# Optimization experiments

Measured on AMD Instinct MI355X. Metric: run time of the kernel, lower is better.

The kernel has to match this reference:

```python
import jax, jax.numpy as jnp
import numpy as np
import math

N_EMBED = 1024
N_HEAD = 16
BLOCK_SIZE = 2048

def setup_inputs() -> dict:
    key = jax.random.key(0)
    k1, k2, k3, k4, k5 = jax.random.split(key, 5)
    s = 0.02
    x = jax.random.normal(k1, (2, 2048, N_EMBED), dtype=jnp.float32)
    W_qkv = jax.random.normal(k2, (N_EMBED, 3 * N_EMBED), dtype=jnp.float32) * s
    b_qkv = jax.random.normal(k3, (3 * N_EMBED,), dtype=jnp.float32) * s
    W_out = jax.random.normal(k4, (N_EMBED, N_EMBED), dtype=jnp.float32) * s
    b_out = jax.random.normal(k5, (N_EMBED,), dtype=jnp.float32) * s
    return {"x": x, "W_qkv": W_qkv, "b_qkv": b_qkv, "W_out": W_out, "b_out": b_out}

def reference(x, W_qkv, b_qkv, W_out, b_out):
    b, s, d = x.shape
    hd = d // N_HEAD  # head dim
    qkv = x @ W_qkv + b_qkv                       # [b, s, 3d]
    q, k, v = jnp.split(qkv, 3, axis=-1)
    # [b, h, s, hd]
    q = q.reshape(b, s, N_HEAD, hd).transpose(0, 2, 1, 3)
    k = k.reshape(b, s, N_HEAD, hd).transpose(0, 2, 1, 3)
    v = v.reshape(b, s, N_HEAD, hd).transpose(0, 2, 1, 3)
    scale = 1.0 / math.sqrt(hd)
    sims = jnp.einsum('bhqd,bhkd->bhqk', q, k) * scale  # [b, h, s, s]
    causal = jnp.tril(jnp.ones((s, s), dtype=bool))
    sims = jnp.where(causal[None, None], sims, -jnp.inf)
    probs = jax.nn.softmax(sims, axis=-1)
    attn = jnp.einsum('bhqk,bhkd->bhqd', probs, v)       # [b, h, s, hd]
    attn = attn.transpose(0, 2, 1, 3).reshape(b, s, d)
    return attn @ W_out + b_out
```

## Files before the change

kernel.cpp:

```cpp
#include <hip/hip_runtime.h>
#include <hip/hip_bf16.h>

typedef __attribute__((ext_vector_type(8))) short short8;
typedef __attribute__((ext_vector_type(4))) short short4v;
typedef __attribute__((ext_vector_type(4))) float f32x4;
typedef __attribute__((ext_vector_type(16))) float f32x16;
typedef __attribute__((ext_vector_type(4))) unsigned int u32x4;
typedef unsigned short u16;

__device__ __forceinline__ u16 f2bf(float f) {
  __hip_bfloat16 h = __float2bfloat16(f);
  return __builtin_bit_cast(unsigned short, h);
}

__device__ __forceinline__ unsigned pack2(float lo, float hi) {
  return (unsigned)f2bf(lo) | ((unsigned)f2bf(hi) << 16);
}

__device__ __forceinline__ void gload16(const u16* g, u16* l) {
  __builtin_amdgcn_global_load_lds(
      (const __attribute__((address_space(1))) unsigned int*)g,
      (__attribute__((address_space(3))) unsigned int*)l, 16, 0, 0);
}

__global__ void prep_kernel(const float* __restrict__ x,
                            const float* __restrict__ Wqkv,
                            const float* __restrict__ Wout,
                            u16* __restrict__ Xb,
                            u16* __restrict__ WqkvT,
                            u16* __restrict__ WoutT) {
  __shared__ float tile[32][33];
  const int b = blockIdx.x, tid = threadIdx.x;
  if (b < 4096) {
    const int i = (b * 256 + tid) * 4;
    float4 f = *(const float4*)(x + i);
    uint2 pk;
    pk.x = pack2(f.x, f.y);
    pk.y = pack2(f.z, f.w);
    *(uint2*)(Xb + i) = pk;
    return;
  }
  const float* in;
  u16* out;
  int N, bx, by;
  if (b < 7168) {
    in = Wqkv; out = WqkvT; N = 3072;
    const int bb = b - 4096;
    bx = bb % 96; by = bb / 96;
  } else {
    in = Wout; out = WoutT; N = 1024;
    const int bb = b - 7168;
    bx = bb % 32; by = bb / 32;
  }
  const int n0 = bx * 32, k0 = by * 32;
  const int tx = tid & 31, ty = tid >> 5;
#pragma unroll
  for (int r = 0; r < 4; ++r) {
    const int k = ty + r * 8;
    tile[k][tx] = in[(size_t)(k0 + k) * N + n0 + tx];
  }
  __syncthreads();
#pragma unroll
  for (int r = 0; r < 4; ++r) {
    const int n = ty + r * 8;
    out[(size_t)(n0 + n) * 1024 + k0 + tx] = f2bf(tile[tx][n]);
  }
}

template <int EPI, int BN>
__global__ __launch_bounds__(256, 2) void gemm_kernel(const u16* __restrict__ A,
                                                      const u16* __restrict__ Bt,
                                                      const float* __restrict__ bias,
                                                      void* __restrict__ outp) {
  __shared__ u16 Al[128 * 64];
  __shared__ u16 Bl[BN * 64];
  constexpr int NF = BN / 32;
  const int tid = threadIdx.x;
  const int lane = tid & 63, wid = tid >> 6;
  const int l15 = lane & 15, lg = lane >> 4;
  const int wm = wid >> 1, wn = wid & 1;
  const int m0 = blockIdx.y * 128, n0 = blockIdx.x * BN;

  f32x4 acc[4][NF] = {};

  for (int k0 = 0; k0 < 1024; k0 += 64) {
    __syncthreads();
#pragma unroll
    for (int i = 0; i < 4; ++i) {
      const int p = i * 4096 + tid * 16;
      const int row = p >> 7;
      const int lslot = ((p >> 4) & 7) ^ (row & 7);
      gload16(A + (size_t)(m0 + row) * 1024 + k0 + lslot * 8, Al + i * 2048 + wid * 512);
    }
#pragma unroll
    for (int i = 0; i < NF; ++i) {
      const int p = i * 4096 + tid * 16;
      const int row = p >> 7;
      const int lslot = ((p >> 4) & 7) ^ (row & 7);
      gload16(Bt + (size_t)(n0 + row) * 1024 + k0 + lslot * 8, Bl + i * 2048 + wid * 512);
    }
    __syncthreads();
#pragma unroll
    for (int ks = 0; ks < 2; ++ks) {
      short8 af[4], bfr[NF];
#pragma unroll
      for (int m = 0; m < 4; ++m) {
        const int row = wm * 64 + m * 16 + l15;
        af[m] = *(const short8*)((const char*)Al + row * 128 + (((ks * 4 + lg) ^ (row & 7)) << 4));
      }
#pragma unroll
      for (int n = 0; n < NF; ++n) {
        const int row = wn * (BN / 2) + n * 16 + l15;
        bfr[n] = *(const short8*)((const char*)Bl + row * 128 + (((ks * 4 + lg) ^ (row & 7)) << 4));
      }
#pragma unroll
      for (int m = 0; m < 4; ++m)
#pragma unroll
        for (int n = 0; n < NF; ++n)
          acc[m][n] = __builtin_amdgcn_mfma_f32_16x16x32_bf16(af[m], bfr[n], acc[m][n], 0, 0, 0);
    }
  }

  if (EPI == 0) {
    u16* qkv = (u16*)outp;
#pragma unroll
    for (int m = 0; m < 4; ++m)
#pragma unroll
      for (int n = 0; n < NF; ++n) {
        const int gcol = n0 + wn * (BN / 2) + n * 16 + l15;
        const int which = gcol >> 10, dd = gcol & 1023;
        const int h = dd >> 6, hd = dd & 63;
        const float bb = bias[gcol];
        const int grow0 = m0 + wm * 64 + m * 16 + lg * 4;
        const int b = grow0 >> 11, s0 = grow0 & 2047;
        if (which == 2) {
          const int bsub = (s0 >> 2) & 3;
          const int bper = (bsub == 1) ? 2 : (bsub == 2) ? 1 : bsub;
          const int s0p = (s0 & ~15) | (bper << 2);
          short4v pk;
#pragma unroll
          for (int j = 0; j < 4; ++j) pk[j] = (short)f2bf(acc[m][n][j] + bb);
          *(short4v*)(qkv + (size_t)2 * 4194304 + ((size_t)(b * 16 + h) * 64 + hd) * 2048 + s0p) = pk;
        } else {
          const float sc = (which == 0) ? 0.18033688011112042f : 1.0f;
#pragma unroll
          for (int j = 0; j < 4; ++j) {
            float v = (acc[m][n][j] + bb) * sc;
            qkv[(size_t)which * 4194304 + ((size_t)(b * 16 + h) * 2048 + s0 + j) * 64 + hd] = f2bf(v);
          }
        }
      }
  } else {
    float* O = (float*)outp;
#pragma unroll
    for (int m = 0; m < 4; ++m)
#pragma unroll
      for (int n = 0; n < NF; ++n) {
        const int gcol = n0 + wn * (BN / 2) + n * 16 + l15;
        const float bb = bias[gcol];
#pragma unroll
        for (int j = 0; j < 4; ++j) {
          const int grow = m0 + wm * 64 + m * 16 + lg * 4 + j;
          O[(size_t)grow * 1024 + gcol] = acc[m][n][j] + bb;
        }
      }
  }
}

__global__ __launch_bounds__(256, 2) void attn_kernel(const u16* __restrict__ Q,
                                                      const u16* __restrict__ K,
                                                      const u16* __restrict__ VT,
                                                      u16* __restrict__ Aout) {
  const int bh = blockIdx.y;
  const int p = blockIdx.x;
  const int tid = threadIdx.x, lane = tid & 63, wid = tid >> 6;
  const int l31 = lane & 31, h = lane >> 5;
  const int qs = wid & 1, kp = wid >> 1;

  __shared__ __align__(16) char smem[36864];
  u16(*Kl)[4096] = (u16(*)[4096])smem;
  u16(*Vl)[4096] = (u16(*)[4096])(smem + 16384);

  const u16* Qb = Q + (size_t)bh * 2048 * 64;
  const u16* Kb = K + (size_t)bh * 2048 * 64;
  const u16* Vb = VT + (size_t)bh * 64 * 2048;

  const int qA = p * 64 + qs * 32;
  const int qB = (31 - p) * 64 + qs * 32;
  const int R = 32 - p;

  short8 qfA[4], qfB[4];
#pragma unroll
  for (int ks = 0; ks < 4; ++ks) {
    qfA[ks] = *(const short8*)(Qb + (size_t)(qA + l31) * 64 + ks * 16 + h * 8);
    qfB[ks] = *(const short8*)(Qb + (size_t)(qB + l31) * 64 + ks * 16 + h * 8);
  }

  f32x16 accA[2] = {}, accB[2] = {};
  float mA = -1e30f, mB = -1e30f, lA = 0.f, lB = 0.f;

  auto stage = [&](int buf, size_t kb) {
#pragma unroll
    for (int i = 0; i < 2; ++i) {
      const int row = i * 32 + (tid >> 3);
      const int sc = ((tid & 7) ^ (row & 7)) * 8;
      gload16(Kb + (kb + row) * 64 + sc, &Kl[buf][i * 2048 + wid * 512]);
      gload16(Vb + (size_t)row * 2048 + kb + sc, &Vl[buf][i * 2048 + wid * 512]);
    }
  };

  stage(0, 0);
  __syncthreads();

  for (int t = 0; t < R; ++t) {
    const int cur = t & 1;
    if (t + 1 < R) stage(cur ^ 1, (size_t)(t + 1) * 64);

    const int kvbase = t * 64 + kp * 32;
    const bool actB = kvbase <= qB + 31;
    const bool actA = kvbase <= qA + 31;
    if (actB) {
      short8 kf[4], vf[2][2];
      const int krow = kp * 32 + l31;
#pragma unroll
      for (int ks = 0; ks < 4; ++ks)
        kf[ks] = *(const short8*)((const char*)&Kl[cur][0] + krow * 128 +
                                  (((ks * 2 + h) ^ (krow & 7)) << 4));
#pragma unroll
      for (int n = 0; n < 2; ++n)
#pragma unroll
        for (int ks = 0; ks < 2; ++ks) {
          const int row = n * 32 + l31;
          vf[n][ks] = *(const short8*)((const char*)&Vl[cur][0] + row * 128 +
                                       (((kp * 4 + ks * 2 + h) ^ (row & 7)) << 4));
        }

      f32x16 saB = {}, saA = {};
      __builtin_amdgcn_s_setprio(1);
#pragma unroll
      for (int ks = 0; ks < 4; ++ks)
        saB = __builtin_amdgcn_mfma_f32_32x32x16_bf16(kf[ks], qfB[ks], saB, 0, 0, 0);
      if (actA) {
#pragma unroll
        for (int ks = 0; ks < 4; ++ks)
          saA = __builtin_amdgcn_mfma_f32_32x32x16_bf16(kf[ks], qfA[ks], saA, 0, 0, 0);
      }
      __builtin_amdgcn_s_setprio(0);

      auto finish = [&](f32x16& sa, f32x16(&acc)[2], float& m, float& l, int q0) {
        if (kvbase == q0) {
#pragma unroll
          for (int r = 0; r < 16; ++r) {
            const int kvr = (r & 3) + 8 * (r >> 2) + 4 * h;
            if (kvr > l31) sa[r] = -1e30f;
          }
        }
        const float t0 = fmaxf(fmaxf(sa[0], sa[1]), sa[2]);
        const float t1 = fmaxf(fmaxf(sa[3], sa[4]), sa[5]);
        const float t2 = fmaxf(fmaxf(sa[6], sa[7]), sa[8]);
        const float t3 = fmaxf(fmaxf(sa[9], sa[10]), sa[11]);
        const float t4 = fmaxf(fmaxf(sa[12], sa[13]), sa[14]);
        float rm = fmaxf(fmaxf(fmaxf(t0, t1), t2), fmaxf(fmaxf(t3, t4), sa[15]));
        rm = fmaxf(rm, __shfl_xor(rm, 32));
        if (!__all(rm <= m + 5.0f)) {
          const float mn = fmaxf(m, rm);
          const float corr = exp2f(m - mn);
          m = mn;
          l *= corr;
#pragma unroll
          for (int n = 0; n < 2; ++n)
#pragma unroll
            for (int r = 0; r < 16; ++r) acc[n][r] *= corr;
        }
#pragma unroll
        for (int r = 0; r < 16; ++r) sa[r] = exp2f(sa[r] - m);
        float rs = (((sa[0] + sa[1]) + (sa[2] + sa[3])) + ((sa[4] + sa[5]) + (sa[6] + sa[7]))) +
                   (((sa[8] + sa[9]) + (sa[10] + sa[11])) + ((sa[12] + sa[13]) + (sa[14] + sa[15])));
        l += rs + __shfl_xor(rs, 32);
        unsigned c[8];
#pragma unroll
        for (int i = 0; i < 8; ++i) c[i] = pack2(sa[2 * i], sa[2 * i + 1]);
        const short8 pk0 = __builtin_bit_cast(short8, (u32x4){c[0], c[1], c[2], c[3]});
        const short8 pk1 = __builtin_bit_cast(short8, (u32x4){c[4], c[5], c[6], c[7]});
        __builtin_amdgcn_s_setprio(1);
#pragma unroll
        for (int n = 0; n < 2; ++n) {
          acc[n] = __builtin_amdgcn_mfma_f32_32x32x16_bf16(vf[n][0], pk0, acc[n], 0, 0, 0);
          acc[n] = __builtin_amdgcn_mfma_f32_32x32x16_bf16(vf[n][1], pk1, acc[n], 0, 0, 0);
        }
        __builtin_amdgcn_s_setprio(0);
      };

      finish(saB, accB, mB, lB, qB);
      if (actA) finish(saA, accA, mA, lA, qA);
    }
    __syncthreads();
  }

  float* comb = (float*)smem;
  float* pA = comb + ((qs * 2 + 0) * 64 + lane) * 36;
  float* pB = comb + ((qs * 2 + 1) * 64 + lane) * 36;
  if (kp == 1) {
    pA[0] = mA; pA[1] = lA;
    pB[0] = mB; pB[1] = lB;
#pragma unroll
    for (int n = 0; n < 2; ++n)
#pragma unroll
      for (int r = 0; r < 16; ++r) {
        pA[2 + n * 16 + r] = accA[n][r];
        pB[2 + n * 16 + r] = accB[n][r];
      }
  }
  __syncthreads();
  if (kp == 0) {
    const int b = bh >> 4, hh = bh & 15;
    auto merge_store = [&](const float* pp, const f32x16(&acc)[2], float m0, float l0, int q0) {
      const float m1 = pp[0], l1 = pp[1];
      const float mn = fmaxf(m0, m1);
      const float c0 = exp2f(m0 - mn), c1 = exp2f(m1 - mn);
      const float inv = 1.0f / (l0 * c0 + l1 * c1);
      u16* rowp = Aout + (size_t)(b * 2048 + q0 + l31) * 1024 + hh * 64;
#pragma unroll
      for (int n = 0; n < 2; ++n)
#pragma unroll
        for (int r = 0; r < 16; r += 2) {
          const int hd = n * 32 + (r & 3) + 8 * (r >> 2) + 4 * h;
          const float v0 = (acc[n][r] * c0 + pp[2 + n * 16 + r] * c1) * inv;
          const float v1 = (acc[n][r + 1] * c0 + pp[2 + n * 16 + r + 1] * c1) * inv;
          *(unsigned*)(rowp + hd) = pack2(v0, v1);
        }
    };
    merge_store(pA, accA, mA, lA, qA);
    merge_store(pB, accB, mB, lB, qB);
  }
}

extern "C" void kernel_launch(void* const* d_in, const int* in_sizes, int n_in,
                              void* d_out, int out_size, void* d_ws, size_t ws_size,
                              hipStream_t stream) {
  const float* x = (const float*)d_in[0];
  const float* Wqkv = (const float*)d_in[1];
  const float* bqkv = (const float*)d_in[2];
  const float* Wout = (const float*)d_in[3];
  const float* bout = (const float*)d_in[4];

  char* ws = (char*)d_ws;
  u16* Xb = (u16*)(ws + 0);
  u16* WqkvT = (u16*)(ws + 8388608);
  u16* WoutT = (u16*)(ws + 14680064);
  u16* QKV = (u16*)(ws + 16777216);
  u16* Attn = Xb;

  prep_kernel<<<8192, 256, 0, stream>>>(x, Wqkv, Wout, Xb, WqkvT, WoutT);
  gemm_kernel<0, 128><<<dim3(24, 32), 256, 0, stream>>>(Xb, WqkvT, bqkv, QKV);
  attn_kernel<<<dim3(16, 32), 256, 0, stream>>>(QKV, QKV + 4194304, QKV + 8388608, Attn);
  gemm_kernel<1, 64><<<dim3(16, 32), 256, 0, stream>>>(Attn, WoutT, bout, d_out);
}
```

Before: 102.0 us.

## Split attention KV range across four wave pairs with 512-thread blocks

The attention block grows from 256 to 512 threads, so four KV splits (kp 0..3) process two 64-row KV tiles per round instead of two splits over one tile. The loop count per block roughly halves and more waves are available to hide latency. In exchange, shared memory doubles to 64 KB for the double-buffered K/V, and the final softmax merge becomes a three-step serialized reduction with extra barriers. Occupancy may drop because of the larger LDS footprint and register pressure.

New measurement: 272.3 us. +166.9%, slower.

```diff
diff --git a/kernel.cpp b/kernel.cpp
--- a/kernel.cpp
+++ b/kernel.cpp
@@ -167,7 +167,7 @@
   }
 }
 
-__global__ __launch_bounds__(256, 2) void attn_kernel(const u16* __restrict__ Q,
+__global__ __launch_bounds__(512, 4) void attn_kernel(const u16* __restrict__ Q,
                                                       const u16* __restrict__ K,
                                                       const u16* __restrict__ VT,
                                                       u16* __restrict__ Aout) {
@@ -176,10 +176,11 @@
   const int tid = threadIdx.x, lane = tid & 63, wid = tid >> 6;
   const int l31 = lane & 31, h = lane >> 5;
   const int qs = wid & 1, kp = wid >> 1;
-
-  __shared__ __align__(16) char smem[36864];
-  u16(*Kl)[4096] = (u16(*)[4096])smem;
-  u16(*Vl)[4096] = (u16(*)[4096])(smem + 16384);
+  const int jt = kp >> 1, sub = kp & 1;
+
+  __shared__ __align__(16) char smem[65536];
+  u16(*Kl)[8192] = (u16(*)[8192])smem;
+  u16(*Vl)[8192] = (u16(*)[8192])(smem + 32768);
 
   const u16* Qb = Q + (size_t)bh * 2048 * 64;
   const u16* Kb = K + (size_t)bh * 2048 * 64;
@@ -188,6 +189,7 @@
   const int qA = p * 64 + qs * 32;
   const int qB = (31 - p) * 64 + qs * 32;
   const int R = 32 - p;
+  const int ROUNDS = (R + 1) >> 1;
 
   short8 qfA[4], qfB[4];
 #pragma unroll
@@ -199,40 +201,43 @@
   f32x16 accA[2] = {}, accB[2] = {};
   float mA = -1e30f, mB = -1e30f, lA = 0.f, lB = 0.f;
 
-  auto stage = [&](int buf, size_t kb) {
-#pragma unroll
-    for (int i = 0; i < 2; ++i) {
-      const int row = i * 32 + (tid >> 3);
-      const int sc = ((tid & 7) ^ (row & 7)) * 8;
-      gload16(Kb + (kb + row) * 64 + sc, &Kl[buf][i * 2048 + wid * 512]);
-      gload16(Vb + (size_t)row * 2048 + kb + sc, &Vl[buf][i * 2048 + wid * 512]);
+  const int srow = tid >> 3;
+  const int ssc = ((tid & 7) ^ (srow & 7)) * 8;
+  auto stage = [&](int buf, size_t kb, int nt) {
+    for (int i = 0; i < nt; ++i) {
+      gload16(Kb + (kb + i * 64 + srow) * 64 + ssc, &Kl[buf][i * 4096 + wid * 512]);
+      gload16(Vb + (size_t)srow * 2048 + kb + i * 64 + ssc, &Vl[buf][i * 4096 + wid * 512]);
     }
   };
 
-  stage(0, 0);
+  stage(0, 0, (R >= 2) ? 2 : 1);
   __syncthreads();
 
-  for (int t = 0; t < R; ++t) {
-    const int cur = t & 1;
-    if (t + 1 < R) stage(cur ^ 1, (size_t)(t + 1) * 64);
-
-    const int kvbase = t * 64 + kp * 32;
-    const bool actB = kvbase <= qB + 31;
-    const bool actA = kvbase <= qA + 31;
+  for (int r = 0; r < ROUNDS; ++r) {
+    const int cur = r & 1;
+    const int rem = R - 2 * (r + 1);
+    const int ntn = rem >= 2 ? 2 : (rem == 1 ? 1 : 0);
+    if (ntn > 0) stage(cur ^ 1, (size_t)(2 * (r + 1)) * 64, ntn);
+
+    const int kvbase = r * 128 + kp * 32;
+    const bool valid = (4 * r + kp) < 2 * R;
+    const bool actB = valid && kvbase <= qB + 31;
+    const bool actA = valid && kvbase <= qA + 31;
     if (actB) {
+      const char* Klt = (const char*)&Kl[cur][jt * 4096];
+      const char* Vlt = (const char*)&Vl[cur][jt * 4096];
       short8 kf[4], vf[2][2];
-      const int krow = kp * 32 + l31;
+      const int krow = sub * 32 + l31;
 #pragma unroll
       for (int ks = 0; ks < 4; ++ks)
-        kf[ks] = *(const short8*)((const char*)&Kl[cur][0] + krow * 128 +
-                                  (((ks * 2 + h) ^ (krow & 7)) << 4));
+        kf[ks] = *(const short8*)(Klt + krow * 128 + (((ks * 2 + h) ^ (krow & 7)) << 4));
 #pragma unroll
       for (int n = 0; n < 2; ++n)
 #pragma unroll
         for (int ks = 0; ks < 2; ++ks) {
           const int row = n * 32 + l31;
-          vf[n][ks] = *(const short8*)((const char*)&Vl[cur][0] + row * 128 +
-                                       (((kp * 4 + ks * 2 + h) ^ (row & 7)) << 4));
+          vf[n][ks] = *(const short8*)(Vlt + row * 128 +
+                                       (((sub * 4 + ks * 2 + h) ^ (row & 7)) << 4));
         }
 
       f32x16 saB = {}, saA = {};
@@ -250,9 +255,9 @@
       auto finish = [&](f32x16& sa, f32x16(&acc)[2], float& m, float& l, int q0) {
         if (kvbase == q0) {
 #pragma unroll
-          for (int r = 0; r < 16; ++r) {
-            const int kvr = (r & 3) + 8 * (r >> 2) + 4 * h;
-            if (kvr > l31) sa[r] = -1e30f;
+          for (int rr = 0; rr < 16; ++rr) {
+            const int kvr = (rr & 3) + 8 * (rr >> 2) + 4 * h;
+            if (kvr > l31) sa[rr] = -1e30f;
           }
         }
         const float t0 = fmaxf(fmaxf(sa[0], sa[1]), sa[2]);
@@ -270,10 +275,10 @@
 #pragma unroll
           for (int n = 0; n < 2; ++n)
 #pragma unroll
-            for (int r = 0; r < 16; ++r) acc[n][r] *= corr;
-        }
-#pragma unroll
-        for (int r = 0; r < 16; ++r) sa[r] = exp2f(sa[r] - m);
+            for (int rr = 0; rr < 16; ++rr) acc[n][rr] *= corr;
+        }
+#pragma unroll
+        for (int rr = 0; rr < 16; ++rr) sa[rr] = exp2f(sa[rr] - m);
         float rs = (((sa[0] + sa[1]) + (sa[2] + sa[3])) + ((sa[4] + sa[5]) + (sa[6] + sa[7]))) +
                    (((sa[8] + sa[9]) + (sa[10] + sa[11])) + ((sa[12] + sa[13]) + (sa[14] + sa[15])));
         l += rs + __shfl_xor(rs, 32);
@@ -297,41 +302,54 @@
     __syncthreads();
   }
 
-  float* comb = (float*)smem;
-  float* pA = comb + ((qs * 2 + 0) * 64 + lane) * 36;
-  float* pB = comb + ((qs * 2 + 1) * 64 + lane) * 36;
-  if (kp == 1) {
-    pA[0] = mA; pA[1] = lA;
-    pB[0] = mB; pB[1] = lB;
-#pragma unroll
-    for (int n = 0; n < 2; ++n)
-#pragma unroll
-      for (int r = 0; r < 16; ++r) {
-        pA[2 + n * 16 + r] = accA[n][r];
-        pB[2 + n * 16 + r] = accB[n][r];
-      }
-  }
-  __syncthreads();
+  float* pA = (float*)smem + ((qs * 2 + 0) * 64 + lane) * 36;
+  float* pB = (float*)smem + ((qs * 2 + 1) * 64 + lane) * 36;
+  for (int src = 1; src < 4; ++src) {
+    __syncthreads();
+    if (kp == src) {
+      pA[0] = mA; pA[1] = lA;
+      pB[0] = mB; pB[1] = lB;
+#pragma unroll
+      for (int n = 0; n < 2; ++n)
+#pragma unroll
+        for (int r = 0; r < 16; ++r) {
+          pA[2 + n * 16 + r] = accA[n][r];
+          pB[2 + n * 16 + r] = accB[n][r];
+        }
+    }
+    __syncthreads();
+    if (kp == 0) {
+      auto merge = [&](const float* pp, f32x16(&acc)[2], float& m, float& l) {
+        const float m1 = pp[0], l1 = pp[1];
+        const float mn = fmaxf(m, m1);
+        const float c0 = exp2f(m - mn), c1 = exp2f(m1 - mn);
+        l = l * c0 + l1 * c1;
+        m = mn;
+#pragma unroll
+        for (int n = 0; n < 2; ++n)
+#pragma unroll
+          for (int r = 0; r < 16; ++r)
+            acc[n][r] = acc[n][r] * c0 + pp[2 + n * 16 + r] * c1;
+      };
+      merge(pA, accA, mA, lA);
+      merge(pB, accB, mB, lB);
+    }
+  }
   if (kp == 0) {
     const int b = bh >> 4, hh = bh & 15;
-    auto merge_store = [&](const float* pp, const f32x16(&acc)[2], float m0, float l0, int q0) {
-      const float m1 = pp[0], l1 = pp[1];
-      const float mn = fmaxf(m0, m1);
-      const float c0 = exp2f(m0 - mn), c1 = exp2f(m1 - mn);
-      const float inv = 1.0f / (l0 * c0 + l1 * c1);
+    auto store = [&](const f32x16(&acc)[2], float l, int q0) {
+      const float inv = 1.0f / l;
       u16* rowp = Aout + (size_t)(b * 2048 + q0 + l31) * 1024 + hh * 64;
 #pragma unroll
       for (int n = 0; n < 2; ++n)
 #pragma unroll
         for (int r = 0; r < 16; r += 2) {
           const int hd = n * 32 + (r & 3) + 8 * (r >> 2) + 4 * h;
-          const float v0 = (acc[n][r] * c0 + pp[2 + n * 16 + r] * c1) * inv;
-          const float v1 = (acc[n][r + 1] * c0 + pp[2 + n * 16 + r + 1] * c1) * inv;
-          *(unsigned*)(rowp + hd) = pack2(v0, v1);
+          *(unsigned*)(rowp + hd) = pack2(acc[n][r] * inv, acc[n][r + 1] * inv);
         }
     };
-    merge_store(pA, accA, mA, lA, qA);
-    merge_store(pB, accB, mB, lB, qB);
+    store(accA, lA, qA);
+    store(accB, lB, qB);
   }
 }
 
@@ -353,6 +371,6 @@
 
   prep_kernel<<<8192, 256, 0, stream>>>(x, Wqkv, Wout, Xb, WqkvT, WoutT);
   gemm_kernel<0, 128><<<dim3(24, 32), 256, 0, stream>>>(Xb, WqkvT, bqkv, QKV);
-  attn_kernel<<<dim3(16, 32), 256, 0, stream>>>(QKV, QKV + 4194304, QKV + 8388608, Attn);
+  attn_kernel<<<dim3(16, 32), 512, 0, stream>>>(QKV, QKV + 4194304, QKV + 8388608, Attn);
   gemm_kernel<1, 64><<<dim3(16, 32), 256, 0, stream>>>(Attn, WoutT, bout, d_out);
 }
```

## Split attention workgroup into 8 waves, each handling one query tile

Applied to the files above, without the earlier changes.

The attention kernel now launches 512 threads per block instead of 256. The two paired query tiles (early and late causal tiles) are handed to separate wave groups instead of each wave processing both. K/V staging is spread over the 8 waves with one load each, and the final split-KV merge is indexed per tile. The goal is to cut per-wave serial work and register pressure so more waves hide latency. The cost is imbalance: waves on the early tile idle through most iterations while still hitting every barrier, and 8 waves share the same LDS double buffer.

New measurement: 100.2 us. About the same (-1.8%).

```diff
diff --git a/kernel.cpp b/kernel.cpp
--- a/kernel.cpp
+++ b/kernel.cpp
@@ -167,7 +167,7 @@
   }
 }
 
-__global__ __launch_bounds__(256, 2) void attn_kernel(const u16* __restrict__ Q,
+__global__ __launch_bounds__(512, 4) void attn_kernel(const u16* __restrict__ Q,
                                                       const u16* __restrict__ K,
                                                       const u16* __restrict__ VT,
                                                       u16* __restrict__ Aout) {
@@ -175,7 +175,7 @@
   const int p = blockIdx.x;
   const int tid = threadIdx.x, lane = tid & 63, wid = tid >> 6;
   const int l31 = lane & 31, h = lane >> 5;
-  const int qs = wid & 1, kp = wid >> 1;
+  const int tl = wid >> 2, qs = (wid >> 1) & 1, kp = wid & 1;
 
   __shared__ __align__(16) char smem[36864];
   u16(*Kl)[4096] = (u16(*)[4096])smem;
@@ -185,28 +185,23 @@
   const u16* Kb = K + (size_t)bh * 2048 * 64;
   const u16* Vb = VT + (size_t)bh * 64 * 2048;
 
-  const int qA = p * 64 + qs * 32;
-  const int qB = (31 - p) * 64 + qs * 32;
+  const int tile = tl ? p : (31 - p);
+  const int q0 = tile * 64 + qs * 32;
   const int R = 32 - p;
 
-  short8 qfA[4], qfB[4];
-#pragma unroll
-  for (int ks = 0; ks < 4; ++ks) {
-    qfA[ks] = *(const short8*)(Qb + (size_t)(qA + l31) * 64 + ks * 16 + h * 8);
-    qfB[ks] = *(const short8*)(Qb + (size_t)(qB + l31) * 64 + ks * 16 + h * 8);
-  }
-
-  f32x16 accA[2] = {}, accB[2] = {};
-  float mA = -1e30f, mB = -1e30f, lA = 0.f, lB = 0.f;
-
+  short8 qf[4];
+#pragma unroll
+  for (int ks = 0; ks < 4; ++ks)
+    qf[ks] = *(const short8*)(Qb + (size_t)(q0 + l31) * 64 + ks * 16 + h * 8);
+
+  f32x16 acc[2] = {};
+  float m = -1e30f, l = 0.f;
+
+  const int srow = tid >> 3;
+  const int ssc = ((tid & 7) ^ (srow & 7)) * 8;
   auto stage = [&](int buf, size_t kb) {
-#pragma unroll
-    for (int i = 0; i < 2; ++i) {
-      const int row = i * 32 + (tid >> 3);
-      const int sc = ((tid & 7) ^ (row & 7)) * 8;
-      gload16(Kb + (kb + row) * 64 + sc, &Kl[buf][i * 2048 + wid * 512]);
-      gload16(Vb + (size_t)row * 2048 + kb + sc, &Vl[buf][i * 2048 + wid * 512]);
-    }
+    gload16(Kb + (kb + srow) * 64 + ssc, &Kl[buf][wid * 512]);
+    gload16(Vb + (size_t)srow * 2048 + kb + ssc, &Vl[buf][wid * 512]);
   };
 
   stage(0, 0);
@@ -217,9 +212,7 @@
     if (t + 1 < R) stage(cur ^ 1, (size_t)(t + 1) * 64);
 
     const int kvbase = t * 64 + kp * 32;
-    const bool actB = kvbase <= qB + 31;
-    const bool actA = kvbase <= qA + 31;
-    if (actB) {
+    if (kvbase <= q0 + 31) {
       short8 kf[4], vf[2][2];
       const int krow = kp * 32 + l31;
 #pragma unroll
@@ -235,103 +228,83 @@
                                        (((kp * 4 + ks * 2 + h) ^ (row & 7)) << 4));
         }
 
-      f32x16 saB = {}, saA = {};
+      f32x16 sa = {};
       __builtin_amdgcn_s_setprio(1);
 #pragma unroll
       for (int ks = 0; ks < 4; ++ks)
-        saB = __builtin_amdgcn_mfma_f32_32x32x16_bf16(kf[ks], qfB[ks], saB, 0, 0, 0);
-      if (actA) {
-#pragma unroll
-        for (int ks = 0; ks < 4; ++ks)
-          saA = __builtin_amdgcn_mfma_f32_32x32x16_bf16(kf[ks], qfA[ks], saA, 0, 0, 0);
-      }
+        sa = __builtin_amdgcn_mfma_f32_32x32x16_bf16(kf[ks], qf[ks], sa, 0, 0, 0);
       __builtin_amdgcn_s_setprio(0);
 
-      auto finish = [&](f32x16& sa, f32x16(&acc)[2], float& m, float& l, int q0) {
-        if (kvbase == q0) {
-#pragma unroll
-          for (int r = 0; r < 16; ++r) {
-            const int kvr = (r & 3) + 8 * (r >> 2) + 4 * h;
-            if (kvr > l31) sa[r] = -1e30f;
-          }
+      if (kvbase == q0) {
+#pragma unroll
+        for (int r = 0; r < 16; ++r) {
+          const int kvr = (r & 3) + 8 * (r >> 2) + 4 * h;
+          if (kvr > l31) sa[r] = -1e30f;
         }
-        const float t0 = fmaxf(fmaxf(sa[0], sa[1]), sa[2]);
-        const float t1 = fmaxf(fmaxf(sa[3], sa[4]), sa[5]);
-        const float t2 = fmaxf(fmaxf(sa[6], sa[7]), sa[8]);
-        const float t3 = fmaxf(fmaxf(sa[9], sa[10]), sa[11]);
-        const float t4 = fmaxf(fmaxf(sa[12], sa[13]), sa[14]);
-        float rm = fmaxf(fmaxf(fmaxf(t0, t1), t2), fmaxf(fmaxf(t3, t4), sa[15]));
-        rm = fmaxf(rm, __shfl_xor(rm, 32));
-        if (!__all(rm <= m + 5.0f)) {
-          const float mn = fmaxf(m, rm);
-          const float corr = exp2f(m - mn);
-          m = mn;
-          l *= corr;
-#pragma unroll
-          for (int n = 0; n < 2; ++n)
-#pragma unroll
-            for (int r = 0; r < 16; ++r) acc[n][r] *= corr;
-        }
-#pragma unroll
-        for (int r = 0; r < 16; ++r) sa[r] = exp2f(sa[r] - m);
-        float rs = (((sa[0] + sa[1]) + (sa[2] + sa[3])) + ((sa[4] + sa[5]) + (sa[6] + sa[7]))) +
-                   (((sa[8] + sa[9]) + (sa[10] + sa[11])) + ((sa[12] + sa[13]) + (sa[14] + sa[15])));
-        l += rs + __shfl_xor(rs, 32);
-        unsigned c[8];
-#pragma unroll
-        for (int i = 0; i < 8; ++i) c[i] = pack2(sa[2 * i], sa[2 * i + 1]);
-        const short8 pk0 = __builtin_bit_cast(short8, (u32x4){c[0], c[1], c[2], c[3]});
-        const short8 pk1 = __builtin_bit_cast(short8, (u32x4){c[4], c[5], c[6], c[7]});
-        __builtin_amdgcn_s_setprio(1);
-#pragma unroll
-        for (int n = 0; n < 2; ++n) {
-          acc[n] = __builtin_amdgcn_mfma_f32_32x32x16_bf16(vf[n][0], pk0, acc[n], 0, 0, 0);
-          acc[n] = __builtin_amdgcn_mfma_f32_32x32x16_bf16(vf[n][1], pk1, acc[n], 0, 0, 0);
-        }
-        __builtin_amdgcn_s_setprio(0);
-      };
-
-      finish(saB, accB, mB, lB, qB);
-      if (actA) finish(saA, accA, mA, lA, qA);
+      }
+      const float t0 = fmaxf(fmaxf(sa[0], sa[1]), sa[2]);
+      const float t1 = fmaxf(fmaxf(sa[3], sa[4]), sa[5]);
+      const float t2 = fmaxf(fmaxf(sa[6], sa[7]), sa[8]);
+      const float t3 = fmaxf(fmaxf(sa[9], sa[10]), sa[11]);
+      const float t4 = fmaxf(fmaxf(sa[12], sa[13]), sa[14]);
+      float rm = fmaxf(fmaxf(fmaxf(t0, t1), t2), fmaxf(fmaxf(t3, t4), sa[15]));
+      rm = fmaxf(rm, __shfl_xor(rm, 32));
+      if (!__all(rm <= m + 5.0f)) {
+        const float mn = fmaxf(m, rm);
+        const float corr = exp2f(m - mn);
+        m = mn;
+        l *= corr;
+#pragma unroll
+        for (int n = 0; n < 2; ++n)
+#pragma unroll
+          for (int r = 0; r < 16; ++r) acc[n][r] *= corr;
+      }
+#pragma unroll
+      for (int r = 0; r < 16; ++r) sa[r] = exp2f(sa[r] - m);
+      float rs = (((sa[0] + sa[1]) + (sa[2] + sa[3])) + ((sa[4] + sa[5]) + (sa[6] + sa[7]))) +
+                 (((sa[8] + sa[9]) + (sa[10] + sa[11])) + ((sa[12] + sa[13]) + (sa[14] + sa[15])));
+      l += rs + __shfl_xor(rs, 32);
+      unsigned c[8];
+#pragma unroll
+      for (int i = 0; i < 8; ++i) c[i] = pack2(sa[2 * i], sa[2 * i + 1]);
+      const short8 pk0 = __builtin_bit_cast(short8, (u32x4){c[0], c[1], c[2], c[3]});
+      const short8 pk1 = __builtin_bit_cast(short8, (u32x4){c[4], c[5], c[6], c[7]});
+      __builtin_amdgcn_s_setprio(1);
+#pragma unroll
+      for (int n = 0; n < 2; ++n) {
+        acc[n] = __builtin_amdgcn_mfma_f32_32x32x16_bf16(vf[n][0], pk0, acc[n], 0, 0, 0);
+        acc[n] = __builtin_amdgcn_mfma_f32_32x32x16_bf16(vf[n][1], pk1, acc[n], 0, 0, 0);
+      }
+      __builtin_amdgcn_s_setprio(0);
     }
     __syncthreads();
   }
 
-  float* comb = (float*)smem;
-  float* pA = comb + ((qs * 2 + 0) * 64 + lane) * 36;
-  float* pB = comb + ((qs * 2 + 1) * 64 + lane) * 36;
+  float* pp = (float*)smem + (((tl << 1) | qs) * 64 + lane) * 36;
   if (kp == 1) {
-    pA[0] = mA; pA[1] = lA;
-    pB[0] = mB; pB[1] = lB;
+    pp[0] = m; pp[1] = l;
 #pragma unroll
     for (int n = 0; n < 2; ++n)
 #pragma unroll
-      for (int r = 0; r < 16; ++r) {
-        pA[2 + n * 16 + r] = accA[n][r];
-        pB[2 + n * 16 + r] = accB[n][r];
-      }
+      for (int r = 0; r < 16; ++r) pp[2 + n * 16 + r] = acc[n][r];
   }
   __syncthreads();
   if (kp == 0) {
     const int b = bh >> 4, hh = bh & 15;
-    auto merge_store = [&](const float* pp, const f32x16(&acc)[2], float m0, float l0, int q0) {
-      const float m1 = pp[0], l1 = pp[1];
-      const float mn = fmaxf(m0, m1);
-      const float c0 = exp2f(m0 - mn), c1 = exp2f(m1 - mn);
-      const float inv = 1.0f / (l0 * c0 + l1 * c1);
-      u16* rowp = Aout + (size_t)(b * 2048 + q0 + l31) * 1024 + hh * 64;
-#pragma unroll
-      for (int n = 0; n < 2; ++n)
-#pragma unroll
-        for (int r = 0; r < 16; r += 2) {
-          const int hd = n * 32 + (r & 3) + 8 * (r >> 2) + 4 * h;
-          const float v0 = (acc[n][r] * c0 + pp[2 + n * 16 + r] * c1) * inv;
-          const float v1 = (acc[n][r + 1] * c0 + pp[2 + n * 16 + r + 1] * c1) * inv;
-          *(unsigned*)(rowp + hd) = pack2(v0, v1);
-        }
-    };
-    merge_store(pA, accA, mA, lA, qA);
-    merge_store(pB, accB, mB, lB, qB);
+    const float m1 = pp[0], l1 = pp[1];
+    const float mn = fmaxf(m, m1);
+    const float c0 = exp2f(m - mn), c1 = exp2f(m1 - mn);
+    const float inv = 1.0f / (l * c0 + l1 * c1);
+    u16* rowp = Aout + (size_t)(b * 2048 + q0 + l31) * 1024 + hh * 64;
+#pragma unroll
+    for (int n = 0; n < 2; ++n)
+#pragma unroll
+      for (int r = 0; r < 16; r += 2) {
+        const int hd = n * 32 + (r & 3) + 8 * (r >> 2) + 4 * h;
+        const float v0 = (acc[n][r] * c0 + pp[2 + n * 16 + r] * c1) * inv;
+        const float v1 = (acc[n][r + 1] * c0 + pp[2 + n * 16 + r + 1] * c1) * inv;
+        *(unsigned*)(rowp + hd) = pack2(v0, v1);
+      }
   }
 }
 
@@ -353,6 +326,6 @@
 
   prep_kernel<<<8192, 256, 0, stream>>>(x, Wqkv, Wout, Xb, WqkvT, WoutT);
   gemm_kernel<0, 128><<<dim3(24, 32), 256, 0, stream>>>(Xb, WqkvT, bqkv, QKV);
-  attn_kernel<<<dim3(16, 32), 256, 0, stream>>>(QKV, QKV + 4194304, QKV + 8388608, Attn);
+  attn_kernel<<<dim3(16, 32), 512, 0, stream>>>(QKV, QKV + 4194304, QKV + 8388608, Attn);
   gemm_kernel<1, 64><<<dim3(16, 32), 256, 0, stream>>>(Attn, WoutT, bout, d_out);
 }
```

## Give each wave private K/V LDS buffers and drop per-iteration block barriers

Applied to the files above, without the earlier changes.

Each of the four waves now stages only the 32-row K/V slice it consumes into its own double-buffered LDS region. It then waits on its own loads with an explicit vmcnt instead of a workgroup __syncthreads every iteration. This removes the block-wide barrier from the attention inner loop and lets waves progress independently. The cost is LDS growing from 36 KB to 64 KB per block, which may limit the two-blocks-per-CU occupancy target, plus duplicated K loads across the qs waves.

Measured after the change: 108.2 us. +6.0%, slower.

```diff
diff --git a/kernel.cpp b/kernel.cpp
--- a/kernel.cpp
+++ b/kernel.cpp
@@ -177,9 +177,8 @@
   const int l31 = lane & 31, h = lane >> 5;
   const int qs = wid & 1, kp = wid >> 1;
 
-  __shared__ __align__(16) char smem[36864];
-  u16(*Kl)[4096] = (u16(*)[4096])smem;
-  u16(*Vl)[4096] = (u16(*)[4096])(smem + 16384);
+  __shared__ __align__(16) char smem[65536];
+  u16* wbase = (u16*)smem + wid * 8192;
 
   const u16* Qb = Q + (size_t)bh * 2048 * 64;
   const u16* Kb = K + (size_t)bh * 2048 * 64;
@@ -199,41 +198,46 @@
   f32x16 accA[2] = {}, accB[2] = {};
   float mA = -1e30f, mB = -1e30f, lA = 0.f, lB = 0.f;
 
-  auto stage = [&](int buf, size_t kb) {
-#pragma unroll
-    for (int i = 0; i < 2; ++i) {
-      const int row = i * 32 + (tid >> 3);
-      const int sc = ((tid & 7) ^ (row & 7)) * 8;
-      gload16(Kb + (kb + row) * 64 + sc, &Kl[buf][i * 2048 + wid * 512]);
-      gload16(Vb + (size_t)row * 2048 + kb + sc, &Vl[buf][i * 2048 + wid * 512]);
-    }
+  auto stage = [&](int buf, int t) {
+    const size_t kb = (size_t)t * 64 + kp * 32;
+    u16* dst = wbase + buf * 4096;
+#pragma unroll
+    for (int i = 0; i < 4; ++i) {
+      const int row = i * 8 + (lane >> 3);
+      const int g = (lane & 7) ^ (row & 7);
+      gload16(Kb + (kb + row) * 64 + g * 8, dst + i * 512);
+    }
+#pragma unroll
+    for (int i = 0; i < 4; ++i)
+      gload16(Vb + (size_t)lane * 2048 + kb + i * 8, dst + 2048 + i * 512);
   };
 
   stage(0, 0);
-  __syncthreads();
 
   for (int t = 0; t < R; ++t) {
     const int cur = t & 1;
-    if (t + 1 < R) stage(cur ^ 1, (size_t)(t + 1) * 64);
+    if (t + 1 < R) {
+      stage(cur ^ 1, t + 1);
+      asm volatile("s_waitcnt vmcnt(8)" ::: "memory");
+    } else {
+      asm volatile("s_waitcnt vmcnt(0)" ::: "memory");
+    }
+    __builtin_amdgcn_sched_barrier(0);
 
     const int kvbase = t * 64 + kp * 32;
     const bool actB = kvbase <= qB + 31;
     const bool actA = kvbase <= qA + 31;
     if (actB) {
+      const u16* cb = wbase + cur * 4096;
       short8 kf[4], vf[2][2];
-      const int krow = kp * 32 + l31;
 #pragma unroll
       for (int ks = 0; ks < 4; ++ks)
-        kf[ks] = *(const short8*)((const char*)&Kl[cur][0] + krow * 128 +
-                                  (((ks * 2 + h) ^ (krow & 7)) << 4));
+        kf[ks] = *(const short8*)(cb + l31 * 64 + (((ks * 2 + h) ^ (l31 & 7)) << 3));
 #pragma unroll
       for (int n = 0; n < 2; ++n)
 #pragma unroll
-        for (int ks = 0; ks < 2; ++ks) {
-          const int row = n * 32 + l31;
-          vf[n][ks] = *(const short8*)((const char*)&Vl[cur][0] + row * 128 +
-                                       (((kp * 4 + ks * 2 + h) ^ (row & 7)) << 4));
-        }
+        for (int ks = 0; ks < 2; ++ks)
+          vf[n][ks] = *(const short8*)(cb + 2048 + (ks * 2 + h) * 512 + (n * 32 + l31) * 8);
 
       f32x16 saB = {}, saA = {};
       __builtin_amdgcn_s_setprio(1);
@@ -294,12 +298,11 @@
       finish(saB, accB, mB, lB, qB);
       if (actA) finish(saA, accA, mA, lA, qA);
     }
-    __syncthreads();
-  }
-
-  float* comb = (float*)smem;
-  float* pA = comb + ((qs * 2 + 0) * 64 + lane) * 36;
-  float* pB = comb + ((qs * 2 + 1) * 64 + lane) * 36;
+  }
+
+  __syncthreads();
+  float* pA = (float*)smem + ((qs * 2 + 0) * 64 + lane) * 36;
+  float* pB = (float*)smem + ((qs * 2 + 1) * 64 + lane) * 36;
   if (kp == 1) {
     pA[0] = mA; pA[1] = lA;
     pB[0] = mB; pB[1] = lB;
```
